# Optimization experiments

Hardware: AMD Instinct MI355X
Metric: run time of the kernel (lower is better)

The kernel has to match this reference:

```python
import jax, jax.numpy as jnp
import numpy as np

F = 32          # number of fields
B = 2048        # batch size
K = 64          # embedding dim
H = 64          # attention hidden size
VOCAB = 100000  # hash_size


def setup_inputs() -> dict:
    key = jax.random.key(0)
    ks = jax.random.split(key, 7)
    x = jax.random.randint(ks[0], (F, B), 0, VOCAB)
    emb_v = jax.random.normal(ks[1], (VOCAB, K), jnp.float32) * 0.05
    at_w = jax.random.normal(ks[2], (K, H), jnp.float32) * 0.1
    at_b = jnp.zeros((H,), jnp.float32)
    at_h = jax.random.normal(ks[3], (H, 1), jnp.float32) * 0.1
    p = jax.random.normal(ks[4], (K, 1), jnp.float32) * 0.1
    w0 = jnp.zeros((), jnp.float32)
    w1 = jax.random.normal(ks[5], (VOCAB, 1), jnp.float32) * 0.05
    return {"x": x, "emb_v": emb_v, "at_w": at_w, "at_b": at_b,
            "at_h": at_h, "p": p, "w0": w0, "w1": w1}


def reference(x, emb_v, at_w, at_b, at_h, p, w0, w1):
    # Embedding lookup: [F, B, K]
    V = emb_v[x]
    # Pairwise interactions: all i<j pairs -> [P, B, K], P = F*(F-1)/2
    iu, ju = np.triu_indices(F, k=1)
    VV = V[iu] * V[ju]                                   # [P, B, K]
    # Attention MLP per pair (no softmax in original code)
    hid = jax.nn.relu(jnp.einsum('pbk,kh->pbh', VV, at_w) + at_b)  # [P, B, H]
    score = jnp.einsum('pbh,ho->pbo', hid, at_h)         # [P, B, 1]
    # Attention-weighted sum pooling over pairs -> [B, K]
    pooled = jnp.sum(VV * score, axis=0)
    # Second-order score
    at_fm_score = pooled @ p                             # [B, 1]
    # First-order FM part: sum over fields of w1 lookups
    fm1 = w0 + jnp.sum(w1[x], axis=0)                    # [B, 1]
    logit = at_fm_score + fm1
    prob = jax.nn.sigmoid(logit)
    return prob
```

## Files before the change

kernel.cpp:

```cpp
#include <hip/hip_runtime.h>
#include <math.h>

#define F      32
#define BATCH  2048
#define K      64
#define H      64
#define NPAIR  496
#define NTROW  31

#define WS_PAIRS_OFF    10240

typedef float    v4f __attribute__((ext_vector_type(4)));
typedef _Float16 v8h __attribute__((ext_vector_type(8)));

__global__ void afm_setup(const float* __restrict__ at_w,
                          const float* __restrict__ p,
                          _Float16* __restrict__ bfrag_ws,
                          int*      __restrict__ pairs_ws)
{
    int idx = blockIdx.x * blockDim.x + threadIdx.x;

    if (idx < 5 * 2 * 64) {
        int nt   = idx >> 7;
        int rem  = idx & 127;
        int kk   = rem >> 6;
        int lane = rem & 63;
        int quad = lane >> 4, c = lane & 15;
        v8h w;
        #pragma unroll
        for (int e = 0; e < 8; ++e) {
            int k = kk * 32 + quad * 8 + e;
            float val = (nt < 4) ? at_w[k * H + nt * 16 + c] : p[k];
            w[e] = (_Float16)val;
        }
        *(v8h*)&bfrag_ws[idx * 8] = w;
    }

    if (idx < NTROW * 16) {
        int tr = idx >> 4, c = idx & 15;
        int pr = tr * 16 + c;
        int i = 0, rem = pr;
        while (rem >= F - 1 - i) { rem -= F - 1 - i; ++i; }
        int j = i + 1 + rem;
        int packed = i | (j << 8);
        #pragma unroll
        for (int q = 0; q < 4; ++q)
            pairs_ws[tr * 64 + q * 16 + c] = packed;
    }
}

__global__ __launch_bounds__(256, 4)
void afm_fwd(const int*   __restrict__ x,
             const float* __restrict__ emb_v,
             const float* __restrict__ at_b,
             const float* __restrict__ at_h,
             const float* __restrict__ w0,
             const float* __restrict__ w1,
             const _Float16* __restrict__ bfrag_ws,
             const int*   __restrict__ pairs_ws,
             float*       __restrict__ out)
{
    __shared__ __align__(16) _Float16 Vsh[F][72];
    __shared__ float fm_sh[F];
    __shared__ float wacc[4];

    const int b    = blockIdx.x;
    const int t    = threadIdx.x;
    const int lane = t & 63;
    const int wv   = t >> 6;
    const int c    = lane & 15;

    v8h bf[5][2];
    #pragma unroll
    for (int nt = 0; nt < 5; ++nt)
        #pragma unroll
        for (int kk = 0; kk < 2; ++kk)
            bf[nt][kk] = *(const v8h*)&bfrag_ws[((nt * 2 + kk) * 64 + lane) * 8];

    int prkNxt = pairs_ws[wv * 64 + lane];

    float ah[4];
    v4f abv[5];
    #pragma unroll
    for (int nt = 0; nt < 4; ++nt) {
        float abn = at_b[nt * 16 + c];
        ah[nt]  = at_h[nt * 16 + c];
        abv[nt] = (v4f){abn, abn, abn, abn};
    }
    abv[4] = (v4f){0.f, 0.f, 0.f, 0.f};

    {
        int f  = t >> 3;
        int cb = (t & 7) * 8;
        int idx = x[f * BATCH + b];
        const float4* src = (const float4*)&emb_v[idx * K + cb];
        float4 a0 = src[0], a1 = src[1];
        v8h w;
        w[0] = (_Float16)a0.x; w[1] = (_Float16)a0.y;
        w[2] = (_Float16)a0.z; w[3] = (_Float16)a0.w;
        w[4] = (_Float16)a1.x; w[5] = (_Float16)a1.y;
        w[6] = (_Float16)a1.z; w[7] = (_Float16)a1.w;
        *(v8h*)&Vsh[f][cb] = w;
    }
    if (t < F) fm_sh[t] = w1[x[t * BATCH + b]];

    __syncthreads();

    float accTot = 0.f;
    const int quad = lane >> 4;

    {
        int pi = prkNxt & 255, pj = (prkNxt >> 8) & 255;
        prkNxt = pairs_ws[(wv + 4) * 64 + lane];
        v8h vi0 = *(const v8h*)&Vsh[pi][quad * 8];
        v8h vj0 = *(const v8h*)&Vsh[pj][quad * 8];
        v8h vi1 = *(const v8h*)&Vsh[pi][32 + quad * 8];
        v8h vj1 = *(const v8h*)&Vsh[pj][32 + quad * 8];

        #pragma unroll
        for (int s = 0; s < 8; ++s) {
            v8h af0 = vi0 * vj0;
            v8h af1 = vi1 * vj1;

            if (s < 7) {
                int npi = prkNxt & 255, npj = (prkNxt >> 8) & 255;
                if (s < 6) {
                    int tr2 = wv + 4 * (s + 2);
                    prkNxt = pairs_ws[(tr2 < NTROW ? tr2 : 0) * 64 + lane];
                }
                vi0 = *(const v8h*)&Vsh[npi][quad * 8];
                vj0 = *(const v8h*)&Vsh[npj][quad * 8];
                vi1 = *(const v8h*)&Vsh[npi][32 + quad * 8];
                vj1 = *(const v8h*)&Vsh[npj][32 + quad * 8];
            }

            v4f acc[5];
            #pragma unroll
            for (int nt = 0; nt < 5; ++nt) {
                v4f a = __builtin_amdgcn_mfma_f32_16x16x32_f16(af0, bf[nt][0], abv[nt], 0, 0, 0);
                acc[nt] = __builtin_amdgcn_mfma_f32_16x16x32_f16(af1, bf[nt][1], a, 0, 0, 0);
            }

            if (wv + 4 * s < NTROW) {
                #pragma unroll
                for (int r = 0; r < 4; ++r) {
                    float sp = 0.f;
                    #pragma unroll
                    for (int nt = 0; nt < 4; ++nt)
                        sp = fmaf(fmaxf(acc[nt][r], 0.f), ah[nt], sp);
                    accTot = fmaf(acc[4][r], sp, accTot);
                }
            }
        }
    }

    accTot += __shfl_xor(accTot, 1);
    accTot += __shfl_xor(accTot, 2);
    accTot += __shfl_xor(accTot, 4);
    accTot += __shfl_xor(accTot, 8);
    accTot += __shfl_xor(accTot, 16);
    accTot += __shfl_xor(accTot, 32);
    if (lane == 0) wacc[wv] = accTot;
    __syncthreads();

    if (t == 0) {
        float fm1 = w0[0];
        #pragma unroll
        for (int f = 0; f < F; ++f) fm1 += fm_sh[f];
        float logit = wacc[0] + wacc[1] + wacc[2] + wacc[3] + fm1;
        out[b] = 1.f / (1.f + expf(-logit));
    }
}

extern "C" void kernel_launch(void* const* d_in, const int* in_sizes, int n_in,
                              void* d_out, int out_size, void* d_ws, size_t ws_size,
                              hipStream_t stream) {
    const int*   x     = (const int*)  d_in[0];
    const float* emb_v = (const float*)d_in[1];
    const float* at_w  = (const float*)d_in[2];
    const float* at_b  = (const float*)d_in[3];
    const float* at_h  = (const float*)d_in[4];
    const float* p     = (const float*)d_in[5];
    const float* w0    = (const float*)d_in[6];
    const float* w1    = (const float*)d_in[7];
    float* out = (float*)d_out;

    _Float16* bfrag_ws = (_Float16*)d_ws;
    int*      pairs_ws = (int*)((char*)d_ws + WS_PAIRS_OFF);

    afm_setup<<<3, 256, 0, stream>>>(at_w, p, bfrag_ws, pairs_ws);
    afm_fwd<<<BATCH, 256, 0, stream>>>(x, emb_v, at_b, at_h, w0, w1,
                                       bfrag_ws, pairs_ws, out);
}
```

Baseline: 99.40 us.

## Process four batch elements per block, one per wave, and drop setup kernel

```diff
diff --git a/kernel.cpp b/kernel.cpp
--- a/kernel.cpp
+++ b/kernel.cpp
@@ -7,77 +7,96 @@
 #define H      64
 #define NPAIR  496
 #define NTROW  31
-
-#define WS_PAIRS_OFF    10240
+#define EPB    4
+#define NBLK   (BATCH / EPB)
 
 typedef float    v4f __attribute__((ext_vector_type(4)));
 typedef _Float16 v8h __attribute__((ext_vector_type(8)));
+typedef __fp16   h2  __attribute__((ext_vector_type(2)));
 
-__global__ void afm_setup(const float* __restrict__ at_w,
-                          const float* __restrict__ p,
-                          _Float16* __restrict__ bfrag_ws,
-                          int*      __restrict__ pairs_ws)
-{
-    int idx = blockIdx.x * blockDim.x + threadIdx.x;
-
-    if (idx < 5 * 2 * 64) {
-        int nt   = idx >> 7;
-        int rem  = idx & 127;
-        int kk   = rem >> 6;
-        int lane = rem & 63;
-        int quad = lane >> 4, c = lane & 15;
-        v8h w;
-        #pragma unroll
-        for (int e = 0; e < 8; ++e) {
-            int k = kk * 32 + quad * 8 + e;
-            float val = (nt < 4) ? at_w[k * H + nt * 16 + c] : p[k];
-            w[e] = (_Float16)val;
-        }
-        *(v8h*)&bfrag_ws[idx * 8] = w;
-    }
-
-    if (idx < NTROW * 16) {
-        int tr = idx >> 4, c = idx & 15;
-        int pr = tr * 16 + c;
-        int i = 0, rem = pr;
-        while (rem >= F - 1 - i) { rem -= F - 1 - i; ++i; }
-        int j = i + 1 + rem;
-        int packed = i | (j << 8);
-        #pragma unroll
-        for (int q = 0; q < 4; ++q)
-            pairs_ws[tr * 64 + q * 16 + c] = packed;
-    }
-}
+union V8H { v8h v; h2 h[4]; };
 
 __global__ __launch_bounds__(256, 4)
 void afm_fwd(const int*   __restrict__ x,
              const float* __restrict__ emb_v,
+             const float* __restrict__ at_w,
              const float* __restrict__ at_b,
              const float* __restrict__ at_h,
+             const float* __restrict__ p,
              const float* __restrict__ w0,
              const float* __restrict__ w1,
-             const _Float16* __restrict__ bfrag_ws,
-             const int*   __restrict__ pairs_ws,
              float*       __restrict__ out)
 {
-    __shared__ __align__(16) _Float16 Vsh[F][72];
-    __shared__ float fm_sh[F];
-    __shared__ float wacc[4];
+    __shared__ __align__(16) _Float16 Vsh[EPB][F][72];
+    __shared__ unsigned short pairs_sh[NPAIR + 16];
+    __shared__ float fm_sh[EPB * F];
 
-    const int b    = blockIdx.x;
     const int t    = threadIdx.x;
     const int lane = t & 63;
     const int wv   = t >> 6;
     const int c    = lane & 15;
+    const int quad = lane >> 4;
+    const int b0   = blockIdx.x * EPB;
+
+    if (t < NPAIR / 2) {
+        #pragma unroll
+        for (int u2 = 0; u2 < 2; ++u2) {
+            int pr = t * 2 + u2;
+            int r  = NPAIR - 1 - pr;
+            int u  = (int)((sqrtf((float)(8 * r + 1)) - 1.0f) * 0.5f);
+            if (u * (u + 1) / 2 > r) --u;
+            if ((u + 1) * (u + 2) / 2 <= r) ++u;
+            int i   = F - 2 - u;
+            int off = r - u * (u + 1) / 2;
+            int j   = F - 1 - off;
+            pairs_sh[pr] = (unsigned short)(i | (j << 8));
+        }
+    }
+
+    {
+        int row  = t >> 1;
+        int elem = row >> 5, f = row & 31, half = t & 1;
+        int idx  = x[f * BATCH + b0 + elem];
+        const float4* src = (const float4*)&emb_v[idx * K + half * 32];
+        #pragma unroll
+        for (int j4 = 0; j4 < 4; ++j4) {
+            float4 a = src[j4 * 2], b = src[j4 * 2 + 1];
+            V8H w;
+            w.h[0] = __builtin_amdgcn_cvt_pkrtz(a.x, a.y);
+            w.h[1] = __builtin_amdgcn_cvt_pkrtz(a.z, a.w);
+            w.h[2] = __builtin_amdgcn_cvt_pkrtz(b.x, b.y);
+            w.h[3] = __builtin_amdgcn_cvt_pkrtz(b.z, b.w);
+            *(v8h*)&Vsh[elem][f][half * 32 + j4 * 8] = w.v;
+        }
+    }
+    if (t < EPB * F) {
+        int elem = t >> 5, f = t & 31;
+        fm_sh[t] = w1[x[f * BATCH + b0 + elem]];
+    }
 
     v8h bf[5][2];
     #pragma unroll
-    for (int nt = 0; nt < 5; ++nt)
+    for (int kk = 0; kk < 2; ++kk) {
         #pragma unroll
-        for (int kk = 0; kk < 2; ++kk)
-            bf[nt][kk] = *(const v8h*)&bfrag_ws[((nt * 2 + kk) * 64 + lane) * 8];
-
-    int prkNxt = pairs_ws[wv * 64 + lane];
+        for (int nt = 0; nt < 4; ++nt) {
+            V8H w;
+            #pragma unroll
+            for (int e = 0; e < 8; e += 2) {
+                int k = kk * 32 + quad * 8 + e;
+                w.h[e >> 1] = __builtin_amdgcn_cvt_pkrtz(
+                    at_w[k * H + nt * 16 + c], at_w[(k + 1) * H + nt * 16 + c]);
+            }
+            bf[nt][kk] = w.v;
+        }
+        float4 p0 = *(const float4*)&p[kk * 32 + quad * 8];
+        float4 p1 = *(const float4*)&p[kk * 32 + quad * 8 + 4];
+        V8H w;
+        w.h[0] = __builtin_amdgcn_cvt_pkrtz(p0.x, p0.y);
+        w.h[1] = __builtin_amdgcn_cvt_pkrtz(p0.z, p0.w);
+        w.h[2] = __builtin_amdgcn_cvt_pkrtz(p1.x, p1.y);
+        w.h[3] = __builtin_amdgcn_cvt_pkrtz(p1.z, p1.w);
+        bf[4][kk] = w.v;
+    }
 
     float ah[4];
     v4f abv[5];
@@ -89,86 +108,58 @@
     }
     abv[4] = (v4f){0.f, 0.f, 0.f, 0.f};
 
-    {
-        int f  = t >> 3;
-        int cb = (t & 7) * 8;
-        int idx = x[f * BATCH + b];
-        const float4* src = (const float4*)&emb_v[idx * K + cb];
-        float4 a0 = src[0], a1 = src[1];
-        v8h w;
-        w[0] = (_Float16)a0.x; w[1] = (_Float16)a0.y;
-        w[2] = (_Float16)a0.z; w[3] = (_Float16)a0.w;
-        w[4] = (_Float16)a1.x; w[5] = (_Float16)a1.y;
-        w[6] = (_Float16)a1.z; w[7] = (_Float16)a1.w;
-        *(v8h*)&Vsh[f][cb] = w;
-    }
-    if (t < F) fm_sh[t] = w1[x[t * BATCH + b]];
-
     __syncthreads();
 
+    const _Float16* Vw = &Vsh[wv][0][0];
     float accTot = 0.f;
-    const int quad = lane >> 4;
 
-    {
-        int pi = prkNxt & 255, pj = (prkNxt >> 8) & 255;
-        prkNxt = pairs_ws[(wv + 4) * 64 + lane];
-        v8h vi0 = *(const v8h*)&Vsh[pi][quad * 8];
-        v8h vj0 = *(const v8h*)&Vsh[pj][quad * 8];
-        v8h vi1 = *(const v8h*)&Vsh[pi][32 + quad * 8];
-        v8h vj1 = *(const v8h*)&Vsh[pj][32 + quad * 8];
+    unsigned short pk = pairs_sh[c];
+    int pi = pk & 255, pj = pk >> 8;
+    v8h vi0 = *(const v8h*)&Vw[pi * 72 + quad * 8];
+    v8h vj0 = *(const v8h*)&Vw[pj * 72 + quad * 8];
+    v8h vi1 = *(const v8h*)&Vw[pi * 72 + 32 + quad * 8];
+    v8h vj1 = *(const v8h*)&Vw[pj * 72 + 32 + quad * 8];
+
+    for (int tr = 0; tr < NTROW; ++tr) {
+        v8h af0 = vi0 * vj0;
+        v8h af1 = vi1 * vj1;
+
+        if (tr < NTROW - 1) {
+            pk = pairs_sh[(tr + 1) * 16 + c];
+            pi = pk & 255; pj = pk >> 8;
+            vi0 = *(const v8h*)&Vw[pi * 72 + quad * 8];
+            vj0 = *(const v8h*)&Vw[pj * 72 + quad * 8];
+            vi1 = *(const v8h*)&Vw[pi * 72 + 32 + quad * 8];
+            vj1 = *(const v8h*)&Vw[pj * 72 + 32 + quad * 8];
+        }
+
+        v4f acc[5];
+        #pragma unroll
+        for (int nt = 0; nt < 5; ++nt) {
+            v4f a = __builtin_amdgcn_mfma_f32_16x16x32_f16(af0, bf[nt][0], abv[nt], 0, 0, 0);
+            acc[nt] = __builtin_amdgcn_mfma_f32_16x16x32_f16(af1, bf[nt][1], a, 0, 0, 0);
+        }
 
         #pragma unroll
-        for (int s = 0; s < 8; ++s) {
-            v8h af0 = vi0 * vj0;
-            v8h af1 = vi1 * vj1;
-
-            if (s < 7) {
-                int npi = prkNxt & 255, npj = (prkNxt >> 8) & 255;
-                if (s < 6) {
-                    int tr2 = wv + 4 * (s + 2);
-                    prkNxt = pairs_ws[(tr2 < NTROW ? tr2 : 0) * 64 + lane];
-                }
-                vi0 = *(const v8h*)&Vsh[npi][quad * 8];
-                vj0 = *(const v8h*)&Vsh[npj][quad * 8];
-                vi1 = *(const v8h*)&Vsh[npi][32 + quad * 8];
-                vj1 = *(const v8h*)&Vsh[npj][32 + quad * 8];
-            }
-
-            v4f acc[5];
+        for (int r = 0; r < 4; ++r) {
+            float sp = 0.f;
             #pragma unroll
-            for (int nt = 0; nt < 5; ++nt) {
-                v4f a = __builtin_amdgcn_mfma_f32_16x16x32_f16(af0, bf[nt][0], abv[nt], 0, 0, 0);
-                acc[nt] = __builtin_amdgcn_mfma_f32_16x16x32_f16(af1, bf[nt][1], a, 0, 0, 0);
-            }
-
-            if (wv + 4 * s < NTROW) {
-                #pragma unroll
-                for (int r = 0; r < 4; ++r) {
-                    float sp = 0.f;
-                    #pragma unroll
-                    for (int nt = 0; nt < 4; ++nt)
-                        sp = fmaf(fmaxf(acc[nt][r], 0.f), ah[nt], sp);
-                    accTot = fmaf(acc[4][r], sp, accTot);
-                }
-            }
+            for (int nt = 0; nt < 4; ++nt)
+                sp = fmaf(fmaxf(acc[nt][r], 0.f), ah[nt], sp);
+            accTot = fmaf(acc[4][r], sp, accTot);
         }
     }
 
+    accTot += (lane < F) ? fm_sh[wv * F + lane] : 0.f;
     accTot += __shfl_xor(accTot, 1);
     accTot += __shfl_xor(accTot, 2);
     accTot += __shfl_xor(accTot, 4);
     accTot += __shfl_xor(accTot, 8);
     accTot += __shfl_xor(accTot, 16);
     accTot += __shfl_xor(accTot, 32);
-    if (lane == 0) wacc[wv] = accTot;
-    __syncthreads();
-
-    if (t == 0) {
-        float fm1 = w0[0];
-        #pragma unroll
-        for (int f = 0; f < F; ++f) fm1 += fm_sh[f];
-        float logit = wacc[0] + wacc[1] + wacc[2] + wacc[3] + fm1;
-        out[b] = 1.f / (1.f + expf(-logit));
+    if (lane == 0) {
+        float logit = accTot + w0[0];
+        out[b0 + wv] = 1.f / (1.f + expf(-logit));
     }
 }
 
@@ -185,10 +176,5 @@
     const float* w1    = (const float*)d_in[7];
     float* out = (float*)d_out;
 
-    _Float16* bfrag_ws = (_Float16*)d_ws;
-    int*      pairs_ws = (int*)((char*)d_ws + WS_PAIRS_OFF);
-
-    afm_setup<<<3, 256, 0, stream>>>(at_w, p, bfrag_ws, pairs_ws);
-    afm_fwd<<<BATCH, 256, 0, stream>>>(x, emb_v, at_b, at_h, w0, w1,
-                                       bfrag_ws, pairs_ws, out);
+    afm_fwd<<<NBLK, 256, 0, stream>>>(x, emb_v, at_w, at_b, at_h, p, w0, w1, out);
 }
```

Result: no change. 98.65 us (-0.8%).
